# Kernel tuning notes

Measured on AMD Instinct MI355X. Metric: run time of the kernel, lower is better.

## Reference

```python
import jax, jax.numpy as jnp
import numpy as np

N_RES = 2_000_000
N_DOM = 2
B_WIN = 100
S_STRIDE = 10
HIDDEN = 128


def _build_windows():
    # Faithful port of the __init__ index construction.
    nb_per_res = B_WIN // S_STRIDE
    balance = B_WIN - S_STRIDE + 1
    start = np.maximum(np.arange(N_RES) + balance - B_WIN, 0)
    start = start // S_STRIDE + (start % S_STRIDE != 0).astype(np.int64)
    bs = start[:, None] + np.arange(nb_per_res)[None, :]
    return bs.astype(np.int32)


def setup_inputs() -> dict:
    key = jax.random.key(0)
    ks = jax.random.split(key, 7)
    bs_per_res = _build_windows()
    nb_windows = int(bs_per_res[-1, -1]) + 1  # 200009
    # weights near 1 (original inits to ones) so products stay well-scaled
    weights = jax.random.uniform(ks[0], (nb_windows, N_DOM), minval=0.5, maxval=1.5, dtype=jnp.float32)
    latent_variables = jax.random.normal(ks[1], (6,), dtype=jnp.float32)
    features = jax.random.normal(ks[2], (2, 50), dtype=jnp.float32)  # replaces torch.randn((2,50))
    W1 = jax.random.normal(ks[3], (53, HIDDEN), dtype=jnp.float32) * 0.1
    b1 = jnp.zeros((HIDDEN,), dtype=jnp.float32)
    W2 = jax.random.normal(ks[4], (HIDDEN, 3), dtype=jnp.float32) * 0.1
    b2 = jnp.zeros((3,), dtype=jnp.float32)
    local_frame = jax.random.normal(ks[5], (3, 3), dtype=jnp.float32)
    atom_absolute_positions = jax.random.normal(ks[6], (3 * N_RES, 3), dtype=jnp.float32)
    return {
        'weights': weights,
        'latent_variables': latent_variables,
        'features': features,
        'W1': W1, 'b1': b1, 'W2': W2, 'b2': b2,
        'local_frame': local_frame,
        'atom_absolute_positions': atom_absolute_positions,
        'bs_per_res': jnp.asarray(bs_per_res),
    }


def multiply_windows_weights(weights, bs_per_res):
    # gather: (N_res, nb_per_res, N_dom); product over the window axis, softmax over domains
    gathered = weights[bs_per_res]
    weights_per_residue = jnp.prod(gathered, axis=1)
    return jax.nn.softmax(weights_per_residue, axis=1)


def reference(weights, latent_variables, features, W1, b1, W2, b2,
              local_frame, atom_absolute_positions, bs_per_res):
    attn = multiply_windows_weights(weights, bs_per_res)  # (N_res, N_dom)
    # features_and_latent: (2, 53)
    fl = jnp.concatenate([features, latent_variables.reshape(2, 3)], axis=1)
    h = jax.nn.relu(fl @ W1 + b1)
    scalars_per_domain = h @ W2 + b2  # (N_dom, 3)
    # deform_structure: note module stores local_frame transposed
    translation_vectors = scalars_per_domain @ local_frame.T  # (N_dom, 3)
    translation_per_residue = attn @ translation_vectors      # (N_res, 3)
    new_atom_positions = atom_absolute_positions + jnp.repeat(translation_per_residue, 3, axis=0)
    return new_atom_positions, attn, translation_per_residue
```

## Files before the change

### kernel.cpp

```cpp
#include <hip/hip_runtime.h>

#define N_RES   2000000
#define HIDDEN  128
#define BLK     256

__global__ __launch_bounds__(BLK, 4) void fused_kernel(
    const float* __restrict__ weights,
    const float* __restrict__ latent,
    const float* __restrict__ features,
    const float* __restrict__ W1,
    const float* __restrict__ b1,
    const float* __restrict__ W2,
    const float* __restrict__ b2,
    const float* __restrict__ lf,
    const float* __restrict__ pos,
    float* __restrict__ out_pos,
    float* __restrict__ out_attn,
    float* __restrict__ out_trans)
{
    __shared__ float h[2][HIDDEN];
    __shared__ float sv[6];
    __shared__ float tvs[6];
    __shared__ __align__(16) float t_lds[3 * BLK];

    const int tid  = threadIdx.x;
    const int r0   = blockIdx.x * BLK;
    const int r    = r0 + tid;
    const int nres = min(BLK, N_RES - r0);
    const int nch  = (9 * nres) >> 2;

    const float4* __restrict__ pos4 = (const float4*)(pos + 9ll * r0);
    float4 pA = make_float4(0.f,0.f,0.f,0.f);
    float4 pB = pA, pC = pA;
    if (tid            < nch) pA = pos4[tid];
    if (tid +     BLK  < nch) pB = pos4[tid + BLK];
    if (tid + 2 * BLK  < nch) pC = pos4[tid + 2 * BLK];

    {
        const int d = tid >> 7, j = tid & 127;
        float acc = b1[j];
        #pragma unroll
        for (int k = 0; k < 50; ++k)
            acc += features[d * 50 + k] * W1[k * HIDDEN + j];
        #pragma unroll
        for (int k = 0; k < 3; ++k)
            acc += latent[d * 3 + k] * W1[(50 + k) * HIDDEN + j];
        h[d][j] = fmaxf(acc, 0.0f);
    }
    __syncthreads();
    {
        const int dd   = tid >> 7;
        const int rest = tid & 127;
        const int c    = rest >> 5;
        const int l    = rest & 31;
        if (c < 3) {
            float a = 0.f;
            #pragma unroll
            for (int m = 0; m < 4; ++m)
                a += h[dd][l + 32 * m] * W2[(l + 32 * m) * 3 + c];
            #pragma unroll
            for (int off = 16; off >= 1; off >>= 1)
                a += __shfl_xor(a, off, 64);
            if (l == 0) sv[dd * 3 + c] = a + b2[c];
        }
    }
    __syncthreads();
    if (tid < 6) {
        const int dd = tid / 3, c = tid % 3;
        float a = 0.f;
        #pragma unroll
        for (int k = 0; k < 3; ++k)
            a += sv[dd * 3 + k] * lf[c * 3 + k];
        tvs[tid] = a;
    }
    __syncthreads();

    float t0 = 0.f, t1 = 0.f, t2 = 0.f;
    if (r < N_RES) {
        const int raw   = max(r - 9, 0);
        const int start = (raw + 9) / 10;
        const float2* wbase = (const float2*)(weights) + start;
        float p0 = 1.0f, p1 = 1.0f;
        #pragma unroll
        for (int j = 0; j < 10; ++j) {
            const float2 w = wbase[j];
            p0 *= w.x;
            p1 *= w.y;
        }
        const float m   = fmaxf(p0, p1);
        const float e0  = __expf(p0 - m);
        const float e1  = __expf(p1 - m);
        const float inv = 1.0f / (e0 + e1);
        const float a0  = e0 * inv;
        const float a1  = e1 * inv;

        ((float2*)out_attn)[r] = make_float2(a0, a1);

        t0 = a0 * tvs[0] + a1 * tvs[3];
        t1 = a0 * tvs[1] + a1 * tvs[4];
        t2 = a0 * tvs[2] + a1 * tvs[5];
    }
    t_lds[3 * tid + 0] = t0;
    t_lds[3 * tid + 1] = t1;
    t_lds[3 * tid + 2] = t2;
    __syncthreads();

    const int ntr = (3 * nres) >> 2;
    if (tid < ntr)
        ((float4*)(out_trans + 3ll * r0))[tid] = ((const float4*)t_lds)[tid];

    float4* __restrict__ o4 = (float4*)(out_pos + 9ll * r0);
    auto addt = [&](float4 v, int c) -> float4 {
        float* vp = (float*)&v;
        const int e = 4 * c;
        #pragma unroll
        for (int k = 0; k < 4; ++k) {
            const int idx = e + k;
            const int rl  = idx / 9;
            int cm = idx - 9 * rl;
            cm = (cm >= 6) ? cm - 6 : ((cm >= 3) ? cm - 3 : cm);
            vp[k] += t_lds[3 * rl + cm];
        }
        return v;
    };
    if (tid            < nch) o4[tid          ] = addt(pA, tid          );
    if (tid +     BLK  < nch) o4[tid +     BLK] = addt(pB, tid +     BLK);
    if (tid + 2 * BLK  < nch) o4[tid + 2 * BLK] = addt(pC, tid + 2 * BLK);
}

extern "C" void kernel_launch(void* const* d_in, const int* in_sizes, int n_in,
                              void* d_out, int out_size, void* d_ws, size_t ws_size,
                              hipStream_t stream) {
    const float* weights  = (const float*)d_in[0];
    const float* latent   = (const float*)d_in[1];
    const float* features = (const float*)d_in[2];
    const float* W1       = (const float*)d_in[3];
    const float* b1       = (const float*)d_in[4];
    const float* W2       = (const float*)d_in[5];
    const float* b2       = (const float*)d_in[6];
    const float* lf       = (const float*)d_in[7];
    const float* pos      = (const float*)d_in[8];

    float* out = (float*)d_out;

    const int blocks = (N_RES + BLK - 1) / BLK;
    fused_kernel<<<blocks, BLK, 0, stream>>>(
        weights, latent, features, W1, b1, W2, b2, lf, pos,
        out,
        out + 18000000,
        out + 22000000);
}
```

Before: 247.5 us.

## Hoist tiny MLP into a separate single-block kernel before the deform kernel

The per-block recomputation of the 2x53x128 MLP and the frame projection moves into a one-block kernel that writes six translation values to workspace. The main kernel then reads those six floats and drops two barriers and about 53 weight loads per thread. The position-index arithmetic in the add step is also simplified to a single divide per float4. This adds a second launch and a serial dependency on a tiny kernel, and removes the occupancy hint from the launch bounds.

```diff
diff --git a/kernel.cpp b/kernel.cpp
--- a/kernel.cpp
+++ b/kernel.cpp
@@ -4,23 +4,59 @@
 #define HIDDEN  128
 #define BLK     256
 
-__global__ __launch_bounds__(BLK, 4) void fused_kernel(
+__global__ void mlp_kernel(const float* __restrict__ latent,
+                           const float* __restrict__ features,
+                           const float* __restrict__ W1,
+                           const float* __restrict__ b1,
+                           const float* __restrict__ W2,
+                           const float* __restrict__ b2,
+                           const float* __restrict__ lf,
+                           float* __restrict__ tv_out)
+{
+    __shared__ float h[2][HIDDEN];
+    __shared__ float s[2][3];
+    const int tid = threadIdx.x;
+    const int d = tid >> 7;
+    const int j = tid & 127;
+
+    float acc = b1[j];
+    #pragma unroll 10
+    for (int k = 0; k < 50; ++k)
+        acc += features[d * 50 + k] * W1[k * HIDDEN + j];
+    #pragma unroll
+    for (int k = 0; k < 3; ++k)
+        acc += latent[d * 3 + k] * W1[(50 + k) * HIDDEN + j];
+    h[d][j] = fmaxf(acc, 0.0f);
+    __syncthreads();
+
+    if (tid < 6) {
+        const int dd = tid / 3, c = tid % 3;
+        float a = b2[c];
+        #pragma unroll 16
+        for (int k = 0; k < HIDDEN; ++k)
+            a += h[dd][k] * W2[k * 3 + c];
+        s[dd][c] = a;
+    }
+    __syncthreads();
+
+    if (tid < 6) {
+        const int dd = tid / 3, c = tid % 3;
+        float a = 0.0f;
+        #pragma unroll
+        for (int k = 0; k < 3; ++k)
+            a += s[dd][k] * lf[c * 3 + k];
+        tv_out[dd * 3 + c] = a;
+    }
+}
+
+__global__ __launch_bounds__(BLK) void deform_kernel(
     const float* __restrict__ weights,
-    const float* __restrict__ latent,
-    const float* __restrict__ features,
-    const float* __restrict__ W1,
-    const float* __restrict__ b1,
-    const float* __restrict__ W2,
-    const float* __restrict__ b2,
-    const float* __restrict__ lf,
     const float* __restrict__ pos,
+    const float* __restrict__ tv,
     float* __restrict__ out_pos,
     float* __restrict__ out_attn,
     float* __restrict__ out_trans)
 {
-    __shared__ float h[2][HIDDEN];
-    __shared__ float sv[6];
-    __shared__ float tvs[6];
     __shared__ __align__(16) float t_lds[3 * BLK];
 
     const int tid  = threadIdx.x;
@@ -30,50 +66,14 @@
     const int nch  = (9 * nres) >> 2;
 
     const float4* __restrict__ pos4 = (const float4*)(pos + 9ll * r0);
-    float4 pA = make_float4(0.f,0.f,0.f,0.f);
+    float4 pA = make_float4(0.f, 0.f, 0.f, 0.f);
     float4 pB = pA, pC = pA;
     if (tid            < nch) pA = pos4[tid];
     if (tid +     BLK  < nch) pB = pos4[tid + BLK];
     if (tid + 2 * BLK  < nch) pC = pos4[tid + 2 * BLK];
 
-    {
-        const int d = tid >> 7, j = tid & 127;
-        float acc = b1[j];
-        #pragma unroll
-        for (int k = 0; k < 50; ++k)
-            acc += features[d * 50 + k] * W1[k * HIDDEN + j];
-        #pragma unroll
-        for (int k = 0; k < 3; ++k)
-            acc += latent[d * 3 + k] * W1[(50 + k) * HIDDEN + j];
-        h[d][j] = fmaxf(acc, 0.0f);
-    }
-    __syncthreads();
-    {
-        const int dd   = tid >> 7;
-        const int rest = tid & 127;
-        const int c    = rest >> 5;
-        const int l    = rest & 31;
-        if (c < 3) {
-            float a = 0.f;
-            #pragma unroll
-            for (int m = 0; m < 4; ++m)
-                a += h[dd][l + 32 * m] * W2[(l + 32 * m) * 3 + c];
-            #pragma unroll
-            for (int off = 16; off >= 1; off >>= 1)
-                a += __shfl_xor(a, off, 64);
-            if (l == 0) sv[dd * 3 + c] = a + b2[c];
-        }
-    }
-    __syncthreads();
-    if (tid < 6) {
-        const int dd = tid / 3, c = tid % 3;
-        float a = 0.f;
-        #pragma unroll
-        for (int k = 0; k < 3; ++k)
-            a += sv[dd * 3 + k] * lf[c * 3 + k];
-        tvs[tid] = a;
-    }
-    __syncthreads();
+    const float tv0 = tv[0], tv1 = tv[1], tv2 = tv[2];
+    const float tv3 = tv[3], tv4 = tv[4], tv5 = tv[5];
 
     float t0 = 0.f, t1 = 0.f, t2 = 0.f;
     if (r < N_RES) {
@@ -96,9 +96,9 @@
 
         ((float2*)out_attn)[r] = make_float2(a0, a1);
 
-        t0 = a0 * tvs[0] + a1 * tvs[3];
-        t1 = a0 * tvs[1] + a1 * tvs[4];
-        t2 = a0 * tvs[2] + a1 * tvs[5];
+        t0 = a0 * tv0 + a1 * tv3;
+        t1 = a0 * tv1 + a1 * tv4;
+        t2 = a0 * tv2 + a1 * tv5;
     }
     t_lds[3 * tid + 0] = t0;
     t_lds[3 * tid + 1] = t1;
@@ -113,13 +113,13 @@
     auto addt = [&](float4 v, int c) -> float4 {
         float* vp = (float*)&v;
         const int e = 4 * c;
+        int rl = e / 9;
+        int cm = e - 9 * rl;
         #pragma unroll
         for (int k = 0; k < 4; ++k) {
-            const int idx = e + k;
-            const int rl  = idx / 9;
-            int cm = idx - 9 * rl;
-            cm = (cm >= 6) ? cm - 6 : ((cm >= 3) ? cm - 3 : cm);
-            vp[k] += t_lds[3 * rl + cm];
+            const int c3 = (cm >= 6) ? cm - 6 : ((cm >= 3) ? cm - 3 : cm);
+            vp[k] += t_lds[3 * rl + c3];
+            if (++cm == 9) { cm = 0; ++rl; }
         }
         return v;
     };
@@ -142,10 +142,13 @@
     const float* pos      = (const float*)d_in[8];
 
     float* out = (float*)d_out;
+    float* tvw = (float*)d_ws;
+
+    mlp_kernel<<<1, 256, 0, stream>>>(latent, features, W1, b1, W2, b2, lf, tvw);
 
     const int blocks = (N_RES + BLK - 1) / BLK;
-    fused_kernel<<<blocks, BLK, 0, stream>>>(
-        weights, latent, features, W1, b1, W2, b2, lf, pos,
+    deform_kernel<<<blocks, BLK, 0, stream>>>(
+        weights, pos, tvw,
         out,
         out + 18000000,
         out + 22000000);
```

Result: faster. 231.0 us (-6.7%).

## Use persistent grid-stride tiles, double-buffered LDS, and nontemporal stores

Applied to the files above, without the earlier changes.

Switches from one block per 256-residue tile to a persistent grid of 2048 blocks that loop over tiles. The small MLP prologue then runs once per block rather than once per tile, and a double-buffered LDS array avoids a second barrier per iteration. All output writes become nontemporal stores to reduce cache pollution, and the per-element index math in the add step is simplified to an incremental counter. The risks are fewer resident waves to hide memory latency, and the removed occupancy hint in the launch bounds may change register allocation.

```diff
diff --git a/kernel.cpp b/kernel.cpp
--- a/kernel.cpp
+++ b/kernel.cpp
@@ -3,8 +3,13 @@
 #define N_RES   2000000
 #define HIDDEN  128
 #define BLK     256
+#define NTILES  7813
+#define GRID    2048
 
-__global__ __launch_bounds__(BLK, 4) void fused_kernel(
+typedef float f32x4 __attribute__((ext_vector_type(4)));
+typedef float f32x2 __attribute__((ext_vector_type(2)));
+
+__global__ __launch_bounds__(BLK) void fused_kernel(
     const float* __restrict__ weights,
     const float* __restrict__ latent,
     const float* __restrict__ features,
@@ -21,20 +26,9 @@
     __shared__ float h[2][HIDDEN];
     __shared__ float sv[6];
     __shared__ float tvs[6];
-    __shared__ __align__(16) float t_lds[3 * BLK];
+    __shared__ __align__(16) float t_lds[2][3 * BLK];
 
-    const int tid  = threadIdx.x;
-    const int r0   = blockIdx.x * BLK;
-    const int r    = r0 + tid;
-    const int nres = min(BLK, N_RES - r0);
-    const int nch  = (9 * nres) >> 2;
-
-    const float4* __restrict__ pos4 = (const float4*)(pos + 9ll * r0);
-    float4 pA = make_float4(0.f,0.f,0.f,0.f);
-    float4 pB = pA, pC = pA;
-    if (tid            < nch) pA = pos4[tid];
-    if (tid +     BLK  < nch) pB = pos4[tid + BLK];
-    if (tid + 2 * BLK  < nch) pC = pos4[tid + 2 * BLK];
+    const int tid = threadIdx.x;
 
     {
         const int d = tid >> 7, j = tid & 127;
@@ -75,57 +69,82 @@
     }
     __syncthreads();
 
-    float t0 = 0.f, t1 = 0.f, t2 = 0.f;
-    if (r < N_RES) {
-        const int raw   = max(r - 9, 0);
-        const int start = (raw + 9) / 10;
-        const float2* wbase = (const float2*)(weights) + start;
-        float p0 = 1.0f, p1 = 1.0f;
-        #pragma unroll
-        for (int j = 0; j < 10; ++j) {
-            const float2 w = wbase[j];
-            p0 *= w.x;
-            p1 *= w.y;
+    const float tv0 = tvs[0], tv1 = tvs[1], tv2 = tvs[2];
+    const float tv3 = tvs[3], tv4 = tvs[4], tv5 = tvs[5];
+
+    int buf = 0;
+    for (int tile = blockIdx.x; tile < NTILES; tile += GRID, buf ^= 1) {
+        const int r0   = tile * BLK;
+        const int r    = r0 + tid;
+        const int nres = min(BLK, N_RES - r0);
+        const int nch  = (9 * nres) >> 2;
+
+        const float4* __restrict__ pos4 = (const float4*)(pos + 9ll * r0);
+        float4 pA = make_float4(0.f, 0.f, 0.f, 0.f);
+        float4 pB = pA, pC = pA;
+        if (tid            < nch) pA = pos4[tid];
+        if (tid +     BLK  < nch) pB = pos4[tid + BLK];
+        if (tid + 2 * BLK  < nch) pC = pos4[tid + 2 * BLK];
+
+        float t0 = 0.f, t1 = 0.f, t2 = 0.f;
+        if (r < N_RES) {
+            const int raw   = max(r - 9, 0);
+            const int start = (raw + 9) / 10;
+            const float2* wbase = (const float2*)(weights) + start;
+            float p0 = 1.0f, p1 = 1.0f;
+            #pragma unroll
+            for (int j = 0; j < 10; ++j) {
+                const float2 w = wbase[j];
+                p0 *= w.x;
+                p1 *= w.y;
+            }
+            const float m   = fmaxf(p0, p1);
+            const float e0  = __expf(p0 - m);
+            const float e1  = __expf(p1 - m);
+            const float inv = 1.0f / (e0 + e1);
+            const float a0  = e0 * inv;
+            const float a1  = e1 * inv;
+
+            f32x2 av; av.x = a0; av.y = a1;
+            __builtin_nontemporal_store(av, (f32x2*)out_attn + r);
+
+            t0 = a0 * tv0 + a1 * tv3;
+            t1 = a0 * tv1 + a1 * tv4;
+            t2 = a0 * tv2 + a1 * tv5;
         }
-        const float m   = fmaxf(p0, p1);
-        const float e0  = __expf(p0 - m);
-        const float e1  = __expf(p1 - m);
-        const float inv = 1.0f / (e0 + e1);
-        const float a0  = e0 * inv;
-        const float a1  = e1 * inv;
+        float* __restrict__ tl = t_lds[buf];
+        tl[3 * tid + 0] = t0;
+        tl[3 * tid + 1] = t1;
+        tl[3 * tid + 2] = t2;
+        __syncthreads();
 
-        ((float2*)out_attn)[r] = make_float2(a0, a1);
+        const int ntr = (3 * nres) >> 2;
+        if (tid < ntr)
+            __builtin_nontemporal_store(((const f32x4*)tl)[tid],
+                                        (f32x4*)(out_trans + 3ll * r0) + tid);
 
-        t0 = a0 * tvs[0] + a1 * tvs[3];
-        t1 = a0 * tvs[1] + a1 * tvs[4];
-        t2 = a0 * tvs[2] + a1 * tvs[5];
+        f32x4* __restrict__ o4 = (f32x4*)(out_pos + 9ll * r0);
+        auto addt = [&](float4 v, int c) -> f32x4 {
+            float* vp = (float*)&v;
+            const int e = 4 * c;
+            int rl = e / 9;
+            int cm = e - 9 * rl;
+            #pragma unroll
+            for (int k = 0; k < 4; ++k) {
+                const int c3 = (cm >= 6) ? cm - 6 : ((cm >= 3) ? cm - 3 : cm);
+                vp[k] += tl[3 * rl + c3];
+                if (++cm == 9) { cm = 0; ++rl; }
+            }
+            f32x4 rv; rv.x = v.x; rv.y = v.y; rv.z = v.z; rv.w = v.w;
+            return rv;
+        };
+        if (tid            < nch)
+            __builtin_nontemporal_store(addt(pA, tid          ), o4 + tid          );
+        if (tid +     BLK  < nch)
+            __builtin_nontemporal_store(addt(pB, tid +     BLK), o4 + tid +     BLK);
+        if (tid + 2 * BLK  < nch)
+            __builtin_nontemporal_store(addt(pC, tid + 2 * BLK), o4 + tid + 2 * BLK);
     }
-    t_lds[3 * tid + 0] = t0;
-    t_lds[3 * tid + 1] = t1;
-    t_lds[3 * tid + 2] = t2;
-    __syncthreads();
-
-    const int ntr = (3 * nres) >> 2;
-    if (tid < ntr)
-        ((float4*)(out_trans + 3ll * r0))[tid] = ((const float4*)t_lds)[tid];
-
-    float4* __restrict__ o4 = (float4*)(out_pos + 9ll * r0);
-    auto addt = [&](float4 v, int c) -> float4 {
-        float* vp = (float*)&v;
-        const int e = 4 * c;
-        #pragma unroll
-        for (int k = 0; k < 4; ++k) {
-            const int idx = e + k;
-            const int rl  = idx / 9;
-            int cm = idx - 9 * rl;
-            cm = (cm >= 6) ? cm - 6 : ((cm >= 3) ? cm - 3 : cm);
-            vp[k] += t_lds[3 * rl + cm];
-        }
-        return v;
-    };
-    if (tid            < nch) o4[tid          ] = addt(pA, tid          );
-    if (tid +     BLK  < nch) o4[tid +     BLK] = addt(pB, tid +     BLK);
-    if (tid + 2 * BLK  < nch) o4[tid + 2 * BLK] = addt(pC, tid + 2 * BLK);
 }
 
 extern "C" void kernel_launch(void* const* d_in, const int* in_sizes, int n_in,
@@ -143,8 +162,7 @@
 
     float* out = (float*)d_out;
 
-    const int blocks = (N_RES + BLK - 1) / BLK;
-    fused_kernel<<<blocks, BLK, 0, stream>>>(
+    fused_kernel<<<GRID, BLK, 0, stream>>>(
         weights, latent, features, W1, b1, W2, b2, lf, pos,
         out,
         out + 18000000,
```

Measured after the change: 234.9 us. 5.1% less time.
